# Kernel tuning notes

Hardware: AMD Instinct MI355X
Metric: run time of the kernel (lower is better)

The kernel has to match this reference:

```python
import jax, jax.numpy as jnp
import numpy as np

B, T, C, H = 4, 2048, 1024, 16
D = C // H  # head dim = 64

def setup_inputs() -> dict:
    key = jax.random.key(0)
    k1, k2, k3 = jax.random.split(key, 3)
    s = 1.0 / np.sqrt(C)
    return {
        "x": jax.random.normal(k1, (B, T, C), dtype=jnp.float32),
        "W_attn": jax.random.normal(k2, (C, 3 * C), dtype=jnp.float32) * s,
        "b_attn": jnp.zeros((3 * C,), dtype=jnp.float32),
        "W_proj": jax.random.normal(k3, (C, C), dtype=jnp.float32) * s,
        "b_proj": jnp.zeros((C,), dtype=jnp.float32),
    }

def reference(x, W_attn, b_attn, W_proj, b_proj):
    qkv = x @ W_attn + b_attn                      # [B,T,3C]
    q, k, v = jnp.split(qkv, 3, axis=-1)
    # [B,T,C] -> [B,H,T,D]
    q = q.reshape(B, T, H, D).transpose(0, 2, 1, 3)
    k = k.reshape(B, T, H, D).transpose(0, 2, 1, 3)
    v = v.reshape(B, T, H, D).transpose(0, 2, 1, 3)
    scale = 1.0 / np.sqrt(D)
    att = jnp.einsum('bhqd,bhkd->bhqk', q, k) * scale   # [B,H,T,T]
    causal = jnp.tril(jnp.ones((T, T), dtype=bool))
    att = jnp.where(causal[None, None], att, jnp.float32(-jnp.inf))
    att = jax.nn.softmax(att, axis=-1)
    y = jnp.einsum('bhqk,bhkd->bhqd', att, v)            # [B,H,T,D]
    y = y.transpose(0, 2, 1, 3).reshape(B, T, C)
    return y @ W_proj + b_proj
```

## Files before the change

### kernel.cpp

```cpp
#include <hip/hip_runtime.h>
#include <cstdint>
#include <cstddef>

typedef __bf16 bf16;
typedef __bf16 bf16x8 __attribute__((ext_vector_type(8)));
typedef __bf16 bf16x4 __attribute__((ext_vector_type(4)));
typedef short  s16x4  __attribute__((ext_vector_type(4)));
typedef float  f32x4  __attribute__((ext_vector_type(4)));

#define MFMA16(a, b, c) __builtin_amdgcn_mfma_f32_16x16x32_bf16((a), (b), (c), 0, 0, 0)

#if __has_builtin(__builtin_amdgcn_mfma_f32_16x16x16bf16_1k)
#define HAVE_K16 1
#else
#define HAVE_K16 0
#endif

#if __has_builtin(__builtin_amdgcn_exp2f)
#define EXP2(x) __builtin_amdgcn_exp2f(x)
#else
#define EXP2(x) exp2f(x)
#endif

constexpr int Bsz = 4;
constexpr int T   = 2048;
constexpr int Cd  = 1024;
constexpr int Hn  = 16;
constexpr int Mrows = Bsz * T;
constexpr int QKV_LD = 3 * Cd;

constexpr float QSCALE = 0.125f * 1.4426950408889634f;

__global__ __launch_bounds__(256) void cvt_f32_bf16(const float* __restrict__ in,
                                                    bf16* __restrict__ out, int n) {
    int i = (blockIdx.x * 256 + threadIdx.x) * 8;
    if (i >= n) return;
    float4 a = *(const float4*)(in + i);
    float4 b = *(const float4*)(in + i + 4);
    bf16x8 o;
    o[0] = (bf16)a.x; o[1] = (bf16)a.y; o[2] = (bf16)a.z; o[3] = (bf16)a.w;
    o[4] = (bf16)b.x; o[5] = (bf16)b.y; o[6] = (bf16)b.z; o[7] = (bf16)b.w;
    *(bf16x8*)(out + i) = o;
}

template <int KDIM, int NDIM>
__global__ __launch_bounds__(256) void transpose_cvt(const float* __restrict__ W,
                                                     bf16* __restrict__ Wt) {
    __shared__ float tile[32][33];
    int k0 = blockIdx.y * 32;
    int n0 = blockIdx.x * 32;
    int tx = threadIdx.x;
    int ty = threadIdx.y;
    #pragma unroll
    for (int r = 0; r < 32; r += 8)
        tile[r + ty][tx] = W[(size_t)(k0 + r + ty) * NDIM + n0 + tx];
    __syncthreads();
    #pragma unroll
    for (int r = 0; r < 32; r += 8)
        Wt[(size_t)(n0 + r + ty) * KDIM + k0 + tx] = (bf16)tile[tx][r + ty];
}

template <int N, bool OUT_BF16>
__global__ __launch_bounds__(256) void gemm_bf16(const bf16* __restrict__ A,
                                                 const bf16* __restrict__ Bt,
                                                 const float* __restrict__ bias,
                                                 void* __restrict__ outp,
                                                 float oscale, int oscale_n) {
    constexpr int K = 1024;
    __shared__ __align__(16) bf16 As[128 * 64];
    __shared__ __align__(16) bf16 Bs[128 * 64];

    const int tid  = threadIdx.x;
    const int w    = tid >> 6;
    const int lane = tid & 63;
    const int wm   = w & 1, wn = w >> 1;
    const int quad = lane >> 4, c16 = lane & 15;

    const int lin = (int)(blockIdx.y * gridDim.x + blockIdx.x);
    const int x8  = lin & 7;
    const int q   = lin >> 3;
    const int m0  = (x8 + 8 * (q & 7)) * 128;
    const int n0  = (q >> 3) * 128;

    const int srow = lane >> 3;
    const int scol = ((lane & 7) ^ srow) * 8;
    const int sw   = c16 & 7;

    f32x4 acc[4][4] = {};

    for (int kt = 0; kt < K / 64; ++kt) {
        const int kk = kt * 64;
        #pragma unroll
        for (int i = 0; i < 4; ++i) {
            const int arow = 32 * w + 8 * i;
            __builtin_amdgcn_global_load_lds(
                (const __attribute__((address_space(1))) void*)(A + (size_t)(m0 + arow + srow) * K + kk + scol),
                (__attribute__((address_space(3))) void*)(&As[arow * 64]),
                16, 0, 0);
            __builtin_amdgcn_global_load_lds(
                (const __attribute__((address_space(1))) void*)(Bt + (size_t)(n0 + arow + srow) * K + kk + scol),
                (__attribute__((address_space(3))) void*)(&Bs[arow * 64]),
                16, 0, 0);
        }
        __syncthreads();

        #pragma unroll
        for (int ks = 0; ks < 2; ++ks) {
            const int go = ((ks * 4 + quad) ^ sw) * 8;
            bf16x8 af[4], bfv[4];
            #pragma unroll
            for (int mb = 0; mb < 4; ++mb)
                af[mb] = *(const bf16x8*)&As[(wm * 64 + mb * 16 + c16) * 64 + go];
            #pragma unroll
            for (int nb = 0; nb < 4; ++nb)
                bfv[nb] = *(const bf16x8*)&Bs[(wn * 64 + nb * 16 + c16) * 64 + go];
            #pragma unroll
            for (int mb = 0; mb < 4; ++mb)
                #pragma unroll
                for (int nb = 0; nb < 4; ++nb)
                    acc[mb][nb] = MFMA16(af[mb], bfv[nb], acc[mb][nb]);
        }
        __syncthreads();
    }

    #pragma unroll
    for (int nb = 0; nb < 4; ++nb) {
        const int n = n0 + wn * 64 + nb * 16 + c16;
        const float bv = bias[n];
        const float sc = (n < oscale_n) ? oscale : 1.0f;
        #pragma unroll
        for (int mb = 0; mb < 4; ++mb) {
            const int mbase = m0 + wm * 64 + mb * 16 + quad * 4;
            #pragma unroll
            for (int r = 0; r < 4; ++r) {
                float v = (acc[mb][nb][r] + bv) * sc;
                if (OUT_BF16)
                    ((bf16*)outp)[(size_t)(mbase + r) * N + n] = (bf16)v;
                else
                    ((float*)outp)[(size_t)(mbase + r) * N + n] = v;
            }
        }
    }
}

__global__ __launch_bounds__(256, 2) void attn_fwd(const bf16* __restrict__ qkv,
                                                   bf16* __restrict__ yp0,
                                                   bf16* __restrict__ yp1,
                                                   bf16* __restrict__ yp2,
                                                   float* __restrict__ lp) {
    __shared__ __align__(16) bf16 Ks2[2][4096];
    __shared__ __align__(16) bf16 Vs[2][64 * 64];
#if !HAVE_K16
    __shared__ __align__(16) bf16 Ps[4][32 * 72];
#endif

    const int x    = blockIdx.x;
    const int xq   = x / 3;
    const int sgl  = x - 3 * xq;
    const int h    = blockIdx.y;
    const int bb   = blockIdx.z;
    const int tid  = threadIdx.x;
    const int w    = tid >> 6;
    const int lane = tid & 63;
    const int quad = lane >> 4, c16 = lane & 15;

    const size_t base = (size_t)(bb * T) * QKV_LD;

    const int g = tid >> 5;
    const int p = tid & 31;

    auto vs_store = [&](bf16* vbuf, const bf16x8& va, const bf16x8& vb) {
        #pragma unroll
        for (int j = 0; j < 8; ++j) {
            union { bf16 hh[2]; uint32_t u; } pk;
            pk.hh[0] = va[j]; pk.hh[1] = vb[j];
            const int row = 8 * g + j;
            *(uint32_t*)&vbuf[row * 64 + (((p >> 1) ^ (row & 15)) << 2) + ((p & 1) << 1)] = pk.u;
        }
    };

    bf16* __restrict__ ydst = (sgl == 0) ? yp0 : ((sgl == 1) ? yp1 : yp2);
    float* __restrict__ ldst = lp + (size_t)sgl * Mrows * Hn;

    for (int ph = 0; ph < 2; ++ph) {
        const int qt = ph ? xq : (15 - xq);
        const int q0 = qt * 128;
        const int rowbase = q0 + w * 32;

        const int n = 2 * qt + 2;
        int f0, f1;
        if (ph == 0) { f0 = (n + 2) / 3; f1 = (n + 1) / 3; }
        else         { f0 = n / 3;       f1 = (n + 1) / 3; }
        const int start = (sgl == 0) ? 0 : ((sgl == 1) ? f0 : f0 + f1);
        const int nkt   = (sgl == 0) ? f0 : ((sgl == 1) ? f1 : n - f0 - f1);

        __syncthreads();

        {
            const int kb = start * 64;
            #pragma unroll
            for (int ii = 0; ii < 2; ++ii) {
                const int i = 2 * w + ii;
                const bf16* gp = qkv + base + (size_t)(kb + 8 * i + (lane & 7)) * QKV_LD + Cd + h * 64 + (lane >> 3) * 8;
                __builtin_amdgcn_global_load_lds(
                    (const __attribute__((address_space(1))) void*)gp,
                    (__attribute__((address_space(3))) void*)(&Ks2[0][i * 512]), 16, 0, 0);
            }
            const bf16* vp = qkv + base + (size_t)(kb + 2 * p) * QKV_LD + 2 * Cd + h * 64 + g * 8;
            bf16x8 va = *(const bf16x8*)vp;
            bf16x8 vb = *(const bf16x8*)(vp + QKV_LD);
            vs_store(Vs[0], va, vb);
        }

        bf16x8 qf[2][2];
        #pragma unroll
        for (int mb = 0; mb < 2; ++mb) {
            const bf16* qp = qkv + base + (size_t)(rowbase + 16 * mb + c16) * QKV_LD + h * 64 + quad * 8;
            qf[mb][0] = *(const bf16x8*)qp;
            qf[mb][1] = *(const bf16x8*)(qp + 32);
        }

        f32x4 yacc[2][4] = {};
        float lsum[2] = {};

        for (int j = 0; j < nkt; ++j) {
            const int cur = j & 1, nxt = cur ^ 1;
            const int k0 = (start + j) * 64;
            __syncthreads();

            bf16x8 va, vb;
            const bool more = (j + 1 < nkt);
            if (more) {
                const int kn = k0 + 64;
                #pragma unroll
                for (int ii = 0; ii < 2; ++ii) {
                    const int i = 2 * w + ii;
                    const bf16* gp = qkv + base + (size_t)(kn + 8 * i + (lane & 7)) * QKV_LD + Cd + h * 64 + (lane >> 3) * 8;
                    __builtin_amdgcn_global_load_lds(
                        (const __attribute__((address_space(1))) void*)gp,
                        (__attribute__((address_space(3))) void*)(&Ks2[nxt][i * 512]), 16, 0, 0);
                }
                const bf16* vp = qkv + base + (size_t)(kn + 2 * p) * QKV_LD + 2 * Cd + h * 64 + g * 8;
                va = *(const bf16x8*)vp;
                vb = *(const bf16x8*)(vp + QKV_LD);
            }

            if (k0 <= rowbase + 31) {
                f32x4 s[2][4] = {};
                #pragma unroll
                for (int ks = 0; ks < 2; ++ks)
                    #pragma unroll
                    for (int blk = 0; blk < 4; ++blk) {
                        const bf16x8 kf = *(const bf16x8*)
                            &Ks2[cur][(2 * blk + (c16 >> 3)) * 512 + (4 * ks + quad) * 64 + (c16 & 7) * 8];
                        #pragma unroll
                        for (int mb = 0; mb < 2; ++mb)
                            s[mb][blk] = MFMA16(kf, qf[mb][ks], s[mb][blk]);
                    }

#if HAVE_K16
                union B4 { bf16x4 v; s16x4 s; } pb[2][4];
#endif
                #pragma unroll
                for (int mb = 0; mb < 2; ++mb) {
                    const int rb = rowbase + 16 * mb;
                    const int qglob = rb + c16;
                    const bool needMask = (k0 + 63 > rb);
                    #pragma unroll
                    for (int blk = 0; blk < 4; ++blk) {
                        #pragma unroll
                        for (int r = 0; r < 4; ++r) {
                            const int key = k0 + blk * 16 + quad * 4 + r;
                            float e = s[mb][blk][r];
                            if (needMask) e = (key > qglob) ? -INFINITY : e;
                            float pv = EXP2(e);
                            lsum[mb] += pv;
#if HAVE_K16
                            pb[mb][blk].v[r] = (bf16)pv;
#else
                            Ps[w][(mb * 16 + c16) * 72 + blk * 16 + quad * 4 + r] = (bf16)pv;
#endif
                        }
                    }
                }

#if HAVE_K16
                #pragma unroll
                for (int blk = 0; blk < 4; ++blk)
                    #pragma unroll
                    for (int d16 = 0; d16 < 4; ++d16) {
                        union B4u { bf16x4 v; s16x4 s; } vf;
                        vf.v = *(const bf16x4*)
                            &Vs[cur][(d16 * 16 + c16) * 64 + ((((blk << 2) | quad) ^ c16) << 2)];
                        #pragma unroll
                        for (int mb = 0; mb < 2; ++mb)
                            yacc[mb][d16] = __builtin_amdgcn_mfma_f32_16x16x16bf16_1k(
                                vf.s, pb[mb][blk].s, yacc[mb][d16], 0, 0, 0);
                    }
#else
                asm volatile("s_waitcnt lgkmcnt(0)" ::: "memory");
                #pragma unroll
                for (int ks = 0; ks < 2; ++ks) {
                    bf16x8 pf0 = *(const bf16x8*)&Ps[w][(0 * 16 + c16) * 72 + ks * 32 + quad * 8];
                    bf16x8 pf1 = *(const bf16x8*)&Ps[w][(1 * 16 + c16) * 72 + ks * 32 + quad * 8];
                    #pragma unroll
                    for (int d16 = 0; d16 < 4; ++d16) {
                        const int row = d16 * 16 + c16;
                        const int g0 = ks * 8 + quad * 2;
                        bf16x4 lo = *(const bf16x4*)&Vs[cur][row * 64 + ((g0 ^ c16) << 2)];
                        bf16x4 hi = *(const bf16x4*)&Vs[cur][row * 64 + (((g0 + 1) ^ c16) << 2)];
                        bf16x8 vfr;
                        vfr[0] = lo[0]; vfr[1] = lo[1]; vfr[2] = lo[2]; vfr[3] = lo[3];
                        vfr[4] = hi[0]; vfr[5] = hi[1]; vfr[6] = hi[2]; vfr[7] = hi[3];
                        yacc[0][d16] = MFMA16(pf0, vfr, yacc[0][d16]);
                        yacc[1][d16] = MFMA16(pf1, vfr, yacc[1][d16]);
                    }
                }
#endif
            }

            if (more)
                vs_store(Vs[nxt], va, vb);
        }

        #pragma unroll
        for (int mb = 0; mb < 2; ++mb) {
            lsum[mb] += __shfl_xor(lsum[mb], 16);
            lsum[mb] += __shfl_xor(lsum[mb], 32);
        }

#if HAVE_K16
        #pragma unroll
        for (int mb = 0; mb < 2; ++mb) {
            const int row = rowbase + 16 * mb + c16;
            bf16* yw = ydst + (size_t)(bb * T + row) * Cd + h * 64;
            #pragma unroll
            for (int d16 = 0; d16 < 4; ++d16) {
                bf16x4 o;
                #pragma unroll
                for (int r = 0; r < 4; ++r)
                    o[r] = (bf16)(yacc[mb][d16][r]);
                *(bf16x4*)(yw + d16 * 16 + quad * 4) = o;
            }
            if (quad == 0)
                ldst[(size_t)(bb * T + row) * Hn + h] = lsum[mb];
        }
#else
        #pragma unroll
        for (int mb = 0; mb < 2; ++mb)
            #pragma unroll
            for (int r = 0; r < 4; ++r) {
                const float lsv = __shfl(lsum[mb], quad * 4 + r);
                const int row = rowbase + 16 * mb + quad * 4 + r;
                bf16* yw = ydst + (size_t)(bb * T + row) * Cd + h * 64;
                #pragma unroll
                for (int d16 = 0; d16 < 4; ++d16)
                    yw[d16 * 16 + c16] = (bf16)(yacc[mb][d16][r]);
                if (c16 == 0)
                    ldst[(size_t)(bb * T + row) * Hn + h] = lsv;
            }
#endif
    }
}

__global__ __launch_bounds__(256) void attn_combine(const bf16* __restrict__ yp0,
                                                    const bf16* __restrict__ yp1,
                                                    const bf16* __restrict__ yp2,
                                                    const float* __restrict__ lp,
                                                    bf16* __restrict__ y) {
    int i = (blockIdx.x * 256 + threadIdx.x) * 8;
    int row = i >> 10;
    int hh  = (i & 1023) >> 6;
    const size_t S = (size_t)Mrows * Hn;
    const size_t li = (size_t)row * Hn + hh;
    float l = lp[li] + lp[S + li] + lp[2 * S + li];
    float inv = 1.f / l;
    bf16x8 a = *(const bf16x8*)(yp0 + i);
    bf16x8 b = *(const bf16x8*)(yp1 + i);
    bf16x8 c = *(const bf16x8*)(yp2 + i);
    bf16x8 o;
    #pragma unroll
    for (int j = 0; j < 8; ++j)
        o[j] = (bf16)(((float)a[j] + (float)b[j] + (float)c[j]) * inv);
    *(bf16x8*)(y + i) = o;
}

extern "C" void kernel_launch(void* const* d_in, const int* in_sizes, int n_in,
                              void* d_out, int out_size, void* d_ws, size_t ws_size,
                              hipStream_t stream) {
    const float* x      = (const float*)d_in[0];
    const float* W_attn = (const float*)d_in[1];
    const float* b_attn = (const float*)d_in[2];
    const float* W_proj = (const float*)d_in[3];
    const float* b_proj = (const float*)d_in[4];
    float* out = (float*)d_out;

    bf16* xb   = (bf16*)d_ws;
    bf16* Wat  = xb  + (size_t)Mrows * Cd;
    bf16* Wpt  = Wat + (size_t)QKV_LD * Cd;
    bf16* qkv  = Wpt + (size_t)Cd * Cd;
    bf16* yb   = qkv + (size_t)Mrows * QKV_LD;
    bf16* yp1  = yb  + (size_t)Mrows * Cd;
    bf16*  yp2 = xb;
    float* lp  = (float*)Wat;

    cvt_f32_bf16<<<(Mrows * Cd) / (256 * 8), 256, 0, stream>>>(x, xb, Mrows * Cd);
    transpose_cvt<Cd, QKV_LD><<<dim3(QKV_LD / 32, Cd / 32), dim3(32, 8), 0, stream>>>(W_attn, Wat);
    transpose_cvt<Cd, Cd><<<dim3(Cd / 32, Cd / 32), dim3(32, 8), 0, stream>>>(W_proj, Wpt);

    gemm_bf16<QKV_LD, true><<<dim3(QKV_LD / 128, Mrows / 128), 256, 0, stream>>>(
        xb, Wat, b_attn, qkv, QSCALE, Cd);

    attn_fwd<<<dim3(24, Hn, Bsz), 256, 0, stream>>>(qkv, yb, yp1, yp2, lp);
    attn_combine<<<(Mrows * Cd) / (256 * 8), 256, 0, stream>>>(yb, yp1, yp2, lp, yb);

    gemm_bf16<Cd, false><<<dim3(Cd / 128, Mrows / 128), 256, 0, stream>>>(
        yb, Wpt, b_proj, out, 1.0f, 0);
}
```

Before: 275.6 us.

## Replace 128x128 GEMM with 256x256 eight-wave pipelined double-buffered kernel

Replaces the 128x128 single-buffered bf16 GEMM with a 256x256 tile kernel using 512 threads (8 waves). It double-buffers the K tiles in 128KB of LDS and interleaves global-to-LDS staging of the next half-tiles with MFMA phases, using partial vmcnt waits and s_setprio. The aim is to hide global load latency and raise arithmetic intensity for both the QKV and output projections. In exchange, the larger tile means fewer blocks (e.g. 64 for the output projection). The hand-scheduled waitcnt and barrier logic is fragile.

```diff
diff --git a/kernel.cpp b/kernel.cpp
--- a/kernel.cpp
+++ b/kernel.cpp
@@ -61,67 +61,101 @@
 }
 
 template <int N, bool OUT_BF16>
-__global__ __launch_bounds__(256) void gemm_bf16(const bf16* __restrict__ A,
-                                                 const bf16* __restrict__ Bt,
-                                                 const float* __restrict__ bias,
-                                                 void* __restrict__ outp,
-                                                 float oscale, int oscale_n) {
-    constexpr int K = 1024;
-    __shared__ __align__(16) bf16 As[128 * 64];
-    __shared__ __align__(16) bf16 Bs[128 * 64];
+__global__ __launch_bounds__(512, 2) void gemm256(const bf16* __restrict__ A,
+                                                  const bf16* __restrict__ Bt,
+                                                  const float* __restrict__ bias,
+                                                  void* __restrict__ outp,
+                                                  float oscale, int oscale_n) {
+    constexpr int K  = 1024;
+    constexpr int KT = K / 64;
+    __shared__ __align__(16) bf16 lds[65536];
 
     const int tid  = threadIdx.x;
-    const int w    = tid >> 6;
+    const int wv   = tid >> 6;
     const int lane = tid & 63;
-    const int wm   = w & 1, wn = w >> 1;
+    const int wm   = wv >> 2;
+    const int wn   = wv & 3;
     const int quad = lane >> 4, c16 = lane & 15;
-
-    const int lin = (int)(blockIdx.y * gridDim.x + blockIdx.x);
+    const int sw   = c16 & 7;
+
+    const int lin = (int)blockIdx.x;
     const int x8  = lin & 7;
     const int q   = lin >> 3;
-    const int m0  = (x8 + 8 * (q & 7)) * 128;
-    const int n0  = (q >> 3) * 128;
-
-    const int srow = lane >> 3;
-    const int scol = ((lane & 7) ^ srow) * 8;
-    const int sw   = c16 & 7;
-
-    f32x4 acc[4][4] = {};
-
-    for (int kt = 0; kt < K / 64; ++kt) {
-        const int kk = kt * 64;
-        #pragma unroll
-        for (int i = 0; i < 4; ++i) {
-            const int arow = 32 * w + 8 * i;
+    const int m0  = (x8 + 8 * (q & 3)) * 256;
+    const int n0  = (q >> 2) * 256;
+
+    auto stage = [&](int kt, int isB, int h, int db) {
+        if (kt >= KT) return;
+        #pragma unroll
+        for (int r = 0; r < 2; ++r) {
+            const int idx  = r * 512 + tid;
+            const int slot = idx >> 3;
+            const int gq   = idx & 7;
+            const int kg   = kt * 64 + ((gq ^ (slot & 7)) << 3);
+            const bf16* src;
+            if (isB) {
+                const int col = ((slot >> 5) << 6) + h * 32 + (slot & 31);
+                src = Bt + (size_t)(n0 + col) * K + kg;
+            } else {
+                const int row = ((slot >> 6) << 7) + h * 64 + (slot & 63);
+                src = A + (size_t)(m0 + row) * K + kg;
+            }
+            bf16* dst = &lds[(isB ? 32768 : 0) + db * 16384 + h * 8192 + (r * 8 + wv) * 512];
             __builtin_amdgcn_global_load_lds(
-                (const __attribute__((address_space(1))) void*)(A + (size_t)(m0 + arow + srow) * K + kk + scol),
-                (__attribute__((address_space(3))) void*)(&As[arow * 64]),
-                16, 0, 0);
-            __builtin_amdgcn_global_load_lds(
-                (const __attribute__((address_space(1))) void*)(Bt + (size_t)(n0 + arow + srow) * K + kk + scol),
-                (__attribute__((address_space(3))) void*)(&Bs[arow * 64]),
-                16, 0, 0);
-        }
-        __syncthreads();
-
-        #pragma unroll
-        for (int ks = 0; ks < 2; ++ks) {
-            const int go = ((ks * 4 + quad) ^ sw) * 8;
-            bf16x8 af[4], bfv[4];
-            #pragma unroll
-            for (int mb = 0; mb < 4; ++mb)
-                af[mb] = *(const bf16x8*)&As[(wm * 64 + mb * 16 + c16) * 64 + go];
-            #pragma unroll
-            for (int nb = 0; nb < 4; ++nb)
-                bfv[nb] = *(const bf16x8*)&Bs[(wn * 64 + nb * 16 + c16) * 64 + go];
-            #pragma unroll
-            for (int mb = 0; mb < 4; ++mb)
-                #pragma unroll
-                for (int nb = 0; nb < 4; ++nb)
-                    acc[mb][nb] = MFMA16(af[mb], bfv[nb], acc[mb][nb]);
-        }
-        __syncthreads();
+                (const __attribute__((address_space(1))) void*)src,
+                (__attribute__((address_space(3))) void*)dst, 16, 0, 0);
+        }
+    };
+
+    f32x4 acc[8][4] = {};
+
+#define PHASE(QM, QN, DB, SKT, SISB, SH, SDB)                                    \
+    {                                                                            \
+        bf16x8 af[4][2], bfr[2][2];                                              \
+        _Pragma("unroll") for (int mq = 0; mq < 4; ++mq)                         \
+            _Pragma("unroll") for (int ks = 0; ks < 2; ++ks)                     \
+                af[mq][ks] = *(const bf16x8*)&lds[(DB) * 16384 + (QM) * 8192 +   \
+                    (wm * 64 + mq * 16 + c16) * 64 + (((ks * 4 + quad) ^ sw) << 3)]; \
+        _Pragma("unroll") for (int nq = 0; nq < 2; ++nq)                         \
+            _Pragma("unroll") for (int ks = 0; ks < 2; ++ks)                     \
+                bfr[nq][ks] = *(const bf16x8*)&lds[32768 + (DB) * 16384 + (QN) * 8192 + \
+                    (wn * 32 + nq * 16 + c16) * 64 + (((ks * 4 + quad) ^ sw) << 3)]; \
+        stage((SKT), (SISB), (SH), (SDB));                                       \
+        __builtin_amdgcn_s_barrier();                                            \
+        __builtin_amdgcn_s_setprio(1);                                           \
+        _Pragma("unroll") for (int mq = 0; mq < 4; ++mq)                         \
+            _Pragma("unroll") for (int nq = 0; nq < 2; ++nq)                     \
+                _Pragma("unroll") for (int ks = 0; ks < 2; ++ks)                 \
+                    acc[(QM) * 4 + mq][(QN) * 2 + nq] =                          \
+                        MFMA16(af[mq][ks], bfr[nq][ks],                          \
+                               acc[(QM) * 4 + mq][(QN) * 2 + nq]);               \
+        __builtin_amdgcn_s_setprio(0);                                           \
+        asm volatile("s_waitcnt vmcnt(6) lgkmcnt(0)" ::: "memory");              \
+        __builtin_amdgcn_s_barrier();                                            \
     }
+
+    stage(0, 0, 0, 0);
+    stage(0, 1, 0, 0);
+    stage(0, 0, 1, 0);
+    stage(0, 1, 1, 0);
+    stage(1, 1, 0, 1);
+    asm volatile("s_waitcnt vmcnt(2)" ::: "memory");
+    __builtin_amdgcn_s_barrier();
+
+    for (int it = 0; it < KT / 2; ++it) {
+        const int v  = 2 * it + 1;
+        const int u2 = 2 * it + 2;
+        const int v2 = 2 * it + 3;
+        PHASE(0, 0, 0,  v, 0, 0, 1)
+        PHASE(1, 0, 0,  v, 0, 1, 1)
+        PHASE(0, 1, 0,  v, 1, 1, 1)
+        PHASE(1, 1, 0, u2, 1, 0, 0)
+        PHASE(0, 0, 1, u2, 0, 0, 0)
+        PHASE(1, 0, 1, u2, 0, 1, 0)
+        PHASE(0, 1, 1, u2, 1, 1, 0)
+        PHASE(1, 1, 1, v2, 1, 0, 1)
+    }
+#undef PHASE
 
     #pragma unroll
     for (int nb = 0; nb < 4; ++nb) {
@@ -129,15 +163,15 @@
         const float bv = bias[n];
         const float sc = (n < oscale_n) ? oscale : 1.0f;
         #pragma unroll
-        for (int mb = 0; mb < 4; ++mb) {
-            const int mbase = m0 + wm * 64 + mb * 16 + quad * 4;
+        for (int mb = 0; mb < 8; ++mb) {
+            const int mbase = m0 + wm * 128 + mb * 16 + quad * 4;
             #pragma unroll
             for (int r = 0; r < 4; ++r) {
-                float v = (acc[mb][nb][r] + bv) * sc;
+                float val = (acc[mb][nb][r] + bv) * sc;
                 if (OUT_BF16)
-                    ((bf16*)outp)[(size_t)(mbase + r) * N + n] = (bf16)v;
+                    ((bf16*)outp)[(size_t)(mbase + r) * N + n] = (bf16)val;
                 else
-                    ((float*)outp)[(size_t)(mbase + r) * N + n] = v;
+                    ((float*)outp)[(size_t)(mbase + r) * N + n] = val;
             }
         }
     }
@@ -408,12 +442,12 @@
     transpose_cvt<Cd, QKV_LD><<<dim3(QKV_LD / 32, Cd / 32), dim3(32, 8), 0, stream>>>(W_attn, Wat);
     transpose_cvt<Cd, Cd><<<dim3(Cd / 32, Cd / 32), dim3(32, 8), 0, stream>>>(W_proj, Wpt);
 
-    gemm_bf16<QKV_LD, true><<<dim3(QKV_LD / 128, Mrows / 128), 256, 0, stream>>>(
+    gemm256<QKV_LD, true><<<dim3((Mrows / 256) * (QKV_LD / 256)), dim3(512), 0, stream>>>(
         xb, Wat, b_attn, qkv, QSCALE, Cd);
 
     attn_fwd<<<dim3(24, Hn, Bsz), 256, 0, stream>>>(qkv, yb, yp1, yp2, lp);
     attn_combine<<<(Mrows * Cd) / (256 * 8), 256, 0, stream>>>(yb, yp1, yp2, lp, yb);
 
-    gemm_bf16<Cd, false><<<dim3(Cd / 128, Mrows / 128), 256, 0, stream>>>(
+    gemm256<Cd, false><<<dim3((Mrows / 256) * (Cd / 256)), dim3(512), 0, stream>>>(
         yb, Wpt, b_proj, out, 1.0f, 0);
 }
```

After: 290.4 us. 1.05x slower.

## Replace QKV GEMM with 256x256-tiled, 512-thread, LDS-DMA double-buffered kernel

Applied to the files above, without the earlier changes.

Adds a new bf16 GEMM for the QKV projection that uses 256x256 output tiles computed by 8 waves. Tiles are staged into a 128KB double-buffered LDS region with global_load_lds direct copies and an XOR swizzle. Loads for the next k-tile are interleaved with MFMA quadrants, using s_setprio and partial vmcnt waits to overlap memory with compute, and blocks are remapped so neighbours share A/B tiles in L2. The larger tile cuts global and LDS traffic per FLOP. In exchange it uses far more LDS and registers per block, and it launches only 96 blocks on a device with many CUs, so part of the GPU may sit idle. The epilogue writes scalar, uncoalesced stores.

```diff
diff --git a/kernel.cpp b/kernel.cpp
--- a/kernel.cpp
+++ b/kernel.cpp
@@ -58,6 +58,140 @@
     #pragma unroll
     for (int r = 0; r < 32; r += 8)
         Wt[(size_t)(n0 + r + ty) * KDIM + k0 + tx] = (bf16)tile[tx][r + ty];
+}
+
+template <int N, bool OUT_BF16>
+__global__ __launch_bounds__(512, 2) void gemm256(const bf16* __restrict__ A,
+                                                  const bf16* __restrict__ Bt,
+                                                  const float* __restrict__ bias,
+                                                  void* __restrict__ outp,
+                                                  float oscale, int oscale_n) {
+    constexpr int K  = 1024;
+    constexpr int KT = K / 64;
+    __shared__ __align__(16) bf16 lds[65536];
+
+    const int tid  = threadIdx.x;
+    const int wv   = tid >> 6;
+    const int lane = tid & 63;
+    const int wm   = wv >> 2;
+    const int wn   = wv & 3;
+    const int quad = lane >> 4, c16 = lane & 15;
+    const int sw   = c16 & 7;
+
+    const int lin = (int)blockIdx.x;
+    const int x8  = lin & 7;
+    const int q   = lin >> 3;
+    const int m0  = (x8 + 8 * (q & 3)) * 256;
+    const int n0  = (q >> 2) * 256;
+
+    auto stage = [&](int kt, int isB, int h) {
+        if (kt >= KT) return;
+        const int db = kt & 1;
+        #pragma unroll
+        for (int r = 0; r < 2; ++r) {
+            const int idx  = r * 512 + tid;
+            const int slot = idx >> 3;
+            const int gq   = idx & 7;
+            const int kg   = kt * 64 + ((gq ^ (slot & 7)) << 3);
+            const bf16* src;
+            if (isB) {
+                const int col = ((slot >> 5) << 6) + h * 32 + (slot & 31);
+                src = Bt + (size_t)(n0 + col) * K + kg;
+            } else {
+                const int row = ((slot >> 6) << 7) + h * 64 + (slot & 63);
+                src = A + (size_t)(m0 + row) * K + kg;
+            }
+            bf16* dst = &lds[(isB ? 32768 : 0) + db * 16384 + h * 8192 + (r * 8 + wv) * 512];
+            __builtin_amdgcn_global_load_lds(
+                (const __attribute__((address_space(1))) void*)src,
+                (__attribute__((address_space(3))) void*)dst, 16, 0, 0);
+        }
+    };
+
+    f32x4 acc[8][4] = {};
+    bf16x8 af[4][2], b0[2][2], b1[2][2];
+
+#define READ_A(QM, DB)                                                           \
+    _Pragma("unroll") for (int mq = 0; mq < 4; ++mq)                             \
+        _Pragma("unroll") for (int ks = 0; ks < 2; ++ks)                         \
+            af[mq][ks] = *(const bf16x8*)&lds[(DB) * 16384 + (QM) * 8192 +       \
+                (wm * 64 + mq * 16 + c16) * 64 + (((ks * 4 + quad) ^ sw) << 3)];
+#define READ_B(DST, QN, DB)                                                      \
+    _Pragma("unroll") for (int nq = 0; nq < 2; ++nq)                             \
+        _Pragma("unroll") for (int ks = 0; ks < 2; ++ks)                         \
+            DST[nq][ks] = *(const bf16x8*)&lds[32768 + (DB) * 16384 + (QN) * 8192 + \
+                (wn * 32 + nq * 16 + c16) * 64 + (((ks * 4 + quad) ^ sw) << 3)];
+#define MFMA_Q(QM, QN, BREG)                                                     \
+    __builtin_amdgcn_s_setprio(1);                                               \
+    _Pragma("unroll") for (int mq = 0; mq < 4; ++mq)                             \
+        _Pragma("unroll") for (int nq = 0; nq < 2; ++nq)                         \
+            _Pragma("unroll") for (int ks = 0; ks < 2; ++ks)                     \
+                acc[(QM) * 4 + mq][(QN) * 2 + nq] =                              \
+                    MFMA16(af[mq][ks], BREG[nq][ks],                             \
+                           acc[(QM) * 4 + mq][(QN) * 2 + nq]);                   \
+    __builtin_amdgcn_s_setprio(0);
+#define VMBAR(NSTR)                                                              \
+    asm volatile("s_waitcnt vmcnt(" NSTR ")" ::: "memory");                      \
+    __builtin_amdgcn_s_barrier();
+
+    stage(0, 0, 0); stage(0, 1, 0); stage(0, 1, 1); stage(0, 0, 1);
+    VMBAR("4")
+
+    #pragma unroll 1
+    for (int u = 0; u < KT - 1; ++u) {
+        const int db = u & 1;
+        const int kn = u + 1;
+        READ_A(0, db)
+        READ_B(b0, 0, db)
+        stage(kn, 0, 0); stage(kn, 1, 0);
+        MFMA_Q(0, 0, b0)
+        VMBAR("6")
+        READ_B(b1, 1, db)
+        stage(kn, 1, 1);
+        MFMA_Q(0, 1, b1)
+        VMBAR("6")
+        READ_A(1, db)
+        stage(kn, 0, 1);
+        MFMA_Q(1, 0, b0)
+        __builtin_amdgcn_s_barrier();
+        MFMA_Q(1, 1, b1)
+        VMBAR("4")
+    }
+
+    READ_A(0, 1)
+    READ_B(b0, 0, 1)
+    MFMA_Q(0, 0, b0)
+    VMBAR("2")
+    READ_B(b1, 1, 1)
+    MFMA_Q(0, 1, b1)
+    VMBAR("0")
+    READ_A(1, 1)
+    MFMA_Q(1, 0, b0)
+    MFMA_Q(1, 1, b1)
+
+#undef READ_A
+#undef READ_B
+#undef MFMA_Q
+#undef VMBAR
+
+    #pragma unroll
+    for (int nb = 0; nb < 4; ++nb) {
+        const int n = n0 + wn * 64 + nb * 16 + c16;
+        const float bv = bias[n];
+        const float sc = (n < oscale_n) ? oscale : 1.0f;
+        #pragma unroll
+        for (int mb = 0; mb < 8; ++mb) {
+            const int mbase = m0 + wm * 128 + mb * 16 + quad * 4;
+            #pragma unroll
+            for (int r = 0; r < 4; ++r) {
+                float val = (acc[mb][nb][r] + bv) * sc;
+                if (OUT_BF16)
+                    ((bf16*)outp)[(size_t)(mbase + r) * N + n] = (bf16)val;
+                else
+                    ((float*)outp)[(size_t)(mbase + r) * N + n] = val;
+            }
+        }
+    }
 }
 
 template <int N, bool OUT_BF16>
@@ -408,7 +542,7 @@
     transpose_cvt<Cd, QKV_LD><<<dim3(QKV_LD / 32, Cd / 32), dim3(32, 8), 0, stream>>>(W_attn, Wat);
     transpose_cvt<Cd, Cd><<<dim3(Cd / 32, Cd / 32), dim3(32, 8), 0, stream>>>(W_proj, Wpt);
 
-    gemm_bf16<QKV_LD, true><<<dim3(QKV_LD / 128, Mrows / 128), 256, 0, stream>>>(
+    gemm256<QKV_LD, true><<<dim3((Mrows / 256) * (QKV_LD / 256)), dim3(512), 0, stream>>>(
         xb, Wat, b_attn, qkv, QSCALE, Cd);
 
     attn_fwd<<<dim3(24, Hn, Bsz), 256, 0, stream>>>(qkv, yb, yp1, yp2, lp);
```

New measurement: 272.0 us. About the same (-1.3%).

## Merge prep kernels and use 128x256 triple-buffered pipelined GEMM

Applied to the files above, without the earlier changes.

Fuses the activation conversion and both weight transpose-converts into a single prep launch. Replaces the 128x128 single-buffered GEMM with a 512-thread 128x256 tile kernel. It triple-buffers LDS with async global-to-LDS loads issued ahead of the MFMA work, uses vmcnt-based barriers and raises scheduling priority around the MFMA block. This targets exposed load latency and launch overhead, at the cost of heavy LDS use (144KB) that limits the kernel to one block per CU, plus fewer blocks for the smaller projection GEMM.

```diff
diff --git a/kernel.cpp b/kernel.cpp
--- a/kernel.cpp
+++ b/kernel.cpp
@@ -31,113 +31,151 @@
 
 constexpr float QSCALE = 0.125f * 1.4426950408889634f;
 
-__global__ __launch_bounds__(256) void cvt_f32_bf16(const float* __restrict__ in,
-                                                    bf16* __restrict__ out, int n) {
-    int i = (blockIdx.x * 256 + threadIdx.x) * 8;
-    if (i >= n) return;
-    float4 a = *(const float4*)(in + i);
-    float4 b = *(const float4*)(in + i + 4);
-    bf16x8 o;
-    o[0] = (bf16)a.x; o[1] = (bf16)a.y; o[2] = (bf16)a.z; o[3] = (bf16)a.w;
-    o[4] = (bf16)b.x; o[5] = (bf16)b.y; o[6] = (bf16)b.z; o[7] = (bf16)b.w;
-    *(bf16x8*)(out + i) = o;
-}
-
-template <int KDIM, int NDIM>
-__global__ __launch_bounds__(256) void transpose_cvt(const float* __restrict__ W,
-                                                     bf16* __restrict__ Wt) {
+__global__ __launch_bounds__(256) void prep(const float* __restrict__ x,
+                                            const float* __restrict__ W_attn,
+                                            const float* __restrict__ W_proj,
+                                            bf16* __restrict__ xb,
+                                            bf16* __restrict__ Wat,
+                                            bf16* __restrict__ Wpt) {
     __shared__ float tile[32][33];
-    int k0 = blockIdx.y * 32;
-    int n0 = blockIdx.x * 32;
-    int tx = threadIdx.x;
-    int ty = threadIdx.y;
+    const int bid = blockIdx.x;
+    const int tid = threadIdx.x;
+    if (bid < 4096) {
+        const int i = (bid * 256 + tid) * 8;
+        float4 a = *(const float4*)(x + i);
+        float4 b = *(const float4*)(x + i + 4);
+        bf16x8 o;
+        o[0] = (bf16)a.x; o[1] = (bf16)a.y; o[2] = (bf16)a.z; o[3] = (bf16)a.w;
+        o[4] = (bf16)b.x; o[5] = (bf16)b.y; o[6] = (bf16)b.z; o[7] = (bf16)b.w;
+        *(bf16x8*)(xb + i) = o;
+        return;
+    }
+    const float* W; bf16* Wt; int NDIM, bx, by;
+    if (bid < 4096 + 3072) {
+        const int r = bid - 4096;
+        W = W_attn; Wt = Wat; NDIM = QKV_LD; bx = r % 96; by = r / 96;
+    } else {
+        const int r = bid - 7168;
+        W = W_proj; Wt = Wpt; NDIM = Cd; bx = r & 31; by = r >> 5;
+    }
+    const int k0 = by * 32, n0 = bx * 32;
+    const int tx = tid & 31, ty = tid >> 5;
     #pragma unroll
     for (int r = 0; r < 32; r += 8)
         tile[r + ty][tx] = W[(size_t)(k0 + r + ty) * NDIM + n0 + tx];
     __syncthreads();
     #pragma unroll
     for (int r = 0; r < 32; r += 8)
-        Wt[(size_t)(n0 + r + ty) * KDIM + k0 + tx] = (bf16)tile[tx][r + ty];
+        Wt[(size_t)(n0 + r + ty) * Cd + k0 + tx] = (bf16)tile[tx][r + ty];
 }
 
 template <int N, bool OUT_BF16>
-__global__ __launch_bounds__(256) void gemm_bf16(const bf16* __restrict__ A,
-                                                 const bf16* __restrict__ Bt,
-                                                 const float* __restrict__ bias,
-                                                 void* __restrict__ outp,
-                                                 float oscale, int oscale_n) {
-    constexpr int K = 1024;
-    __shared__ __align__(16) bf16 As[128 * 64];
-    __shared__ __align__(16) bf16 Bs[128 * 64];
+__global__ __launch_bounds__(512, 1) void gemm128x256(const bf16* __restrict__ A,
+                                                      const bf16* __restrict__ Bt,
+                                                      const float* __restrict__ bias,
+                                                      void* __restrict__ outp,
+                                                      float oscale, int oscale_n) {
+    constexpr int K  = 1024;
+    constexpr int KT = 16;
+    __shared__ __align__(16) bf16 lds[73728];
 
     const int tid  = threadIdx.x;
-    const int w    = tid >> 6;
+    const int wv   = tid >> 6;
     const int lane = tid & 63;
-    const int wm   = w & 1, wn = w >> 1;
+    const int wm   = wv >> 2;
+    const int wn   = wv & 3;
     const int quad = lane >> 4, c16 = lane & 15;
-
-    const int lin = (int)(blockIdx.y * gridDim.x + blockIdx.x);
-    const int x8  = lin & 7;
-    const int q   = lin >> 3;
-    const int m0  = (x8 + 8 * (q & 7)) * 128;
-    const int n0  = (q >> 3) * 128;
-
-    const int srow = lane >> 3;
-    const int scol = ((lane & 7) ^ srow) * 8;
     const int sw   = c16 & 7;
 
+    const int lin  = (int)blockIdx.x;
+    const int mIdx = (lin & 7) + 8 * ((lin >> 3) & 7);
+    const int nIdx = lin >> 6;
+    const int m0   = mIdx * 128;
+    const int n0   = nIdx * 256;
+
+    auto stage = [&](int kt) {
+        if (kt >= KT) return;
+        const int db = kt % 3;
+        #pragma unroll
+        for (int r = 0; r < 2; ++r) {
+            const int idx  = r * 512 + tid;
+            const int slot = idx >> 3;
+            const int kg   = kt * 64 + (((idx & 7) ^ (slot & 7)) << 3);
+            __builtin_amdgcn_global_load_lds(
+                (const __attribute__((address_space(1))) void*)(A + (size_t)(m0 + slot) * K + kg),
+                (__attribute__((address_space(3))) void*)(&lds[db * 8192 + (r * 8 + wv) * 512]),
+                16, 0, 0);
+        }
+        #pragma unroll
+        for (int h = 0; h < 2; ++h)
+            #pragma unroll
+            for (int r = 0; r < 2; ++r) {
+                const int idx  = r * 512 + tid;
+                const int slot = idx >> 3;
+                const int kg   = kt * 64 + (((idx & 7) ^ (slot & 7)) << 3);
+                __builtin_amdgcn_global_load_lds(
+                    (const __attribute__((address_space(1))) void*)(Bt + (size_t)(n0 + h * 128 + slot) * K + kg),
+                    (__attribute__((address_space(3))) void*)(&lds[24576 + db * 16384 + h * 8192 + (r * 8 + wv) * 512]),
+                    16, 0, 0);
+            }
+    };
+
     f32x4 acc[4][4] = {};
-
-    for (int kt = 0; kt < K / 64; ++kt) {
-        const int kk = kt * 64;
-        #pragma unroll
-        for (int i = 0; i < 4; ++i) {
-            const int arow = 32 * w + 8 * i;
-            __builtin_amdgcn_global_load_lds(
-                (const __attribute__((address_space(1))) void*)(A + (size_t)(m0 + arow + srow) * K + kk + scol),
-                (__attribute__((address_space(3))) void*)(&As[arow * 64]),
-                16, 0, 0);
-            __builtin_amdgcn_global_load_lds(
-                (const __attribute__((address_space(1))) void*)(Bt + (size_t)(n0 + arow + srow) * K + kk + scol),
-                (__attribute__((address_space(3))) void*)(&Bs[arow * 64]),
-                16, 0, 0);
-        }
-        __syncthreads();
-
-        #pragma unroll
-        for (int ks = 0; ks < 2; ++ks) {
-            const int go = ((ks * 4 + quad) ^ sw) * 8;
-            bf16x8 af[4], bfv[4];
-            #pragma unroll
-            for (int mb = 0; mb < 4; ++mb)
-                af[mb] = *(const bf16x8*)&As[(wm * 64 + mb * 16 + c16) * 64 + go];
-            #pragma unroll
-            for (int nb = 0; nb < 4; ++nb)
-                bfv[nb] = *(const bf16x8*)&Bs[(wn * 64 + nb * 16 + c16) * 64 + go];
-            #pragma unroll
-            for (int mb = 0; mb < 4; ++mb)
-                #pragma unroll
-                for (int nb = 0; nb < 4; ++nb)
-                    acc[mb][nb] = MFMA16(af[mb], bfv[nb], acc[mb][nb]);
-        }
-        __syncthreads();
-    }
+    bf16x8 af[4][2], bfv[4][2];
+
+#define TILE_BODY(DB, SKT)                                                        \
+    {                                                                             \
+        _Pragma("unroll") for (int mq = 0; mq < 4; ++mq)                          \
+            _Pragma("unroll") for (int ks = 0; ks < 2; ++ks)                      \
+                af[mq][ks] = *(const bf16x8*)&lds[(DB) * 8192 +                   \
+                    (wm * 64 + mq * 16 + c16) * 64 + (((ks * 4 + quad) ^ sw) << 3)]; \
+        _Pragma("unroll") for (int nf = 0; nf < 4; ++nf)                          \
+            _Pragma("unroll") for (int ks = 0; ks < 2; ++ks)                      \
+                bfv[nf][ks] = *(const bf16x8*)&lds[24576 + (DB) * 16384 +         \
+                    ((nf >> 1) * 128 + wn * 32 + (nf & 1) * 16 + c16) * 64 +      \
+                    (((ks * 4 + quad) ^ sw) << 3)];                               \
+        stage(SKT);                                                               \
+        __builtin_amdgcn_s_setprio(1);                                            \
+        _Pragma("unroll") for (int mq = 0; mq < 4; ++mq)                          \
+            _Pragma("unroll") for (int nf = 0; nf < 4; ++nf)                      \
+                _Pragma("unroll") for (int ks = 0; ks < 2; ++ks)                  \
+                    acc[mq][nf] = MFMA16(af[mq][ks], bfv[nf][ks], acc[mq][nf]);   \
+        __builtin_amdgcn_s_setprio(0);                                            \
+    }
+#define VMBAR(NSTR)                                                               \
+    asm volatile("s_waitcnt vmcnt(" NSTR ")" ::: "memory");                       \
+    __builtin_amdgcn_s_barrier();
+
+    stage(0);
+    stage(1);
+
+    #pragma unroll 1
+    for (int i = 0; i < 5; ++i) {
+        const int u = 3 * i;
+        VMBAR("6") TILE_BODY(0, u + 2)
+        VMBAR("6") TILE_BODY(1, u + 3)
+        VMBAR("6") TILE_BODY(2, u + 4)
+    }
+    VMBAR("0") TILE_BODY(0, KT)
+
+#undef TILE_BODY
+#undef VMBAR
 
     #pragma unroll
-    for (int nb = 0; nb < 4; ++nb) {
-        const int n = n0 + wn * 64 + nb * 16 + c16;
+    for (int nf = 0; nf < 4; ++nf) {
+        const int n = n0 + (nf >> 1) * 128 + wn * 32 + (nf & 1) * 16 + c16;
         const float bv = bias[n];
         const float sc = (n < oscale_n) ? oscale : 1.0f;
         #pragma unroll
-        for (int mb = 0; mb < 4; ++mb) {
-            const int mbase = m0 + wm * 64 + mb * 16 + quad * 4;
+        for (int mq = 0; mq < 4; ++mq) {
+            const int rowb = m0 + wm * 64 + mq * 16 + quad * 4;
             #pragma unroll
             for (int r = 0; r < 4; ++r) {
-                float v = (acc[mb][nb][r] + bv) * sc;
+                float val = (acc[mq][nf][r] + bv) * sc;
                 if (OUT_BF16)
-                    ((bf16*)outp)[(size_t)(mbase + r) * N + n] = (bf16)v;
+                    ((bf16*)outp)[(size_t)(rowb + r) * N + n] = (bf16)val;
                 else
-                    ((float*)outp)[(size_t)(mbase + r) * N + n] = v;
+                    ((float*)outp)[(size_t)(rowb + r) * N + n] = val;
             }
         }
     }
@@ -404,16 +442,14 @@
     bf16*  yp2 = xb;
     float* lp  = (float*)Wat;
 
-    cvt_f32_bf16<<<(Mrows * Cd) / (256 * 8), 256, 0, stream>>>(x, xb, Mrows * Cd);
-    transpose_cvt<Cd, QKV_LD><<<dim3(QKV_LD / 32, Cd / 32), dim3(32, 8), 0, stream>>>(W_attn, Wat);
-    transpose_cvt<Cd, Cd><<<dim3(Cd / 32, Cd / 32), dim3(32, 8), 0, stream>>>(W_proj, Wpt);
-
-    gemm_bf16<QKV_LD, true><<<dim3(QKV_LD / 128, Mrows / 128), 256, 0, stream>>>(
+    prep<<<8192, 256, 0, stream>>>(x, W_attn, W_proj, xb, Wat, Wpt);
+
+    gemm128x256<QKV_LD, true><<<dim3((Mrows / 128) * (QKV_LD / 256)), dim3(512), 0, stream>>>(
         xb, Wat, b_attn, qkv, QSCALE, Cd);
 
     attn_fwd<<<dim3(24, Hn, Bsz), 256, 0, stream>>>(qkv, yb, yp1, yp2, lp);
     attn_combine<<<(Mrows * Cd) / (256 * 8), 256, 0, stream>>>(yb, yp1, yp2, lp, yb);
 
-    gemm_bf16<Cd, false><<<dim3(Cd / 128, Mrows / 128), 256, 0, stream>>>(
+    gemm128x256<Cd, false><<<dim3((Mrows / 128) * (Cd / 256)), dim3(512), 0, stream>>>(
         yb, Wpt, b_proj, out, 1.0f, 0);
 }
```

Measured after the change: 266.2 us. 1.04x faster.
